# Optimization experiments

Hardware: AMD Instinct MI355X
Metric: run time of the kernel (lower is better)

## Reference

```python
import jax, jax.numpy as jnp
import numpy as np

B, T, H, W = 32, 100, 16, 16
CIN, HID, COUT, K = 64, 128, 64, 5
EPS = 1e-3      # keras LayerNormalization default epsilon
ALPHA = 0.2     # LeakyReLU slope


def _conv_same(x, w):
    # x: [B,H,W,Cin], w: [kh,kw,Cin,Cout] -> [B,H,W,Cout], SAME padding, stride 1
    return jax.lax.conv_general_dilated(
        x, w, window_strides=(1, 1), padding='SAME',
        dimension_numbers=('NHWC', 'HWIO', 'NHWC'))


def setup_inputs() -> dict:
    key = jax.random.key(0)
    ks = jax.random.split(key, 8)
    s = 0.05
    return {
        'initial_input': jax.random.normal(ks[0], (B, 1, H, W, CIN), jnp.float32),
        'h0': jax.random.normal(ks[1], (B, H, W, HID), jnp.float32) * s,
        'c0': jax.random.normal(ks[2], (B, H, W, HID), jnp.float32) * s,
        'targets': jax.random.normal(ks[3], (B, T, H, W, CIN), jnp.float32),
        'autoreg_prob': jnp.float32(0.5),
        # ConvLSTM2D params (keras gate order: i, f, c, o stacked on last axis)
        'Wx': jax.random.normal(ks[4], (K, K, CIN, 4 * HID), jnp.float32) * s,
        'Wh': jax.random.normal(ks[5], (K, K, HID, 4 * HID), jnp.float32) * s,
        'b': jnp.zeros((4 * HID,), jnp.float32),
        # Conv2D(64, 3, same)
        'conv_w': jax.random.normal(ks[6], (3, 3, HID, COUT), jnp.float32) * s,
        'conv_b': jnp.zeros((COUT,), jnp.float32),
        # LayerNorm (axis=-1)
        'gamma': jnp.ones((COUT,), jnp.float32),
        'beta': jnp.zeros((COUT,), jnp.float32),
    }


def reference(initial_input, h0, c0, targets, autoreg_prob,
              Wx, Wh, b, conv_w, conv_b, gamma, beta):
    T_ = targets.shape[1]
    t_switch = jnp.float32(T_) * autoreg_prob
    x0 = initial_input[:, 0]                       # [B,H,W,CIN] (seq-len-1 ConvLSTM step)
    tgt_t = jnp.transpose(targets, (1, 0, 2, 3, 4))  # [T,B,H,W,CIN]
    ts = jnp.arange(T_)

    def step(carry, inp):
        x, h, c = carry
        t, tgt = inp
        # ConvLSTM2D cell (one timestep)
        g = _conv_same(x, Wx) + _conv_same(h, Wh) + b   # [B,H,W,4*HID]
        i_g, f_g, c_g, o_g = jnp.split(g, 4, axis=-1)
        c = jax.nn.sigmoid(f_g) * c + jax.nn.sigmoid(i_g) * jnp.tanh(c_g)
        h = jax.nn.sigmoid(o_g) * jnp.tanh(c)
        # Conv2D -> LayerNorm(axis=-1) -> LeakyReLU(0.2)
        y = _conv_same(h, conv_w) + conv_b              # [B,H,W,COUT]
        mu = jnp.mean(y, axis=-1, keepdims=True)
        var = jnp.var(y, axis=-1, keepdims=True)
        y = (y - mu) * jax.lax.rsqrt(var + EPS) * gamma + beta
        out = jnp.where(y >= 0, y, ALPHA * y)
        # autoreg phase feeds output back; teacher phase feeds targets[:, t]
        next_x = jnp.where(t.astype(jnp.float32) < t_switch, out, tgt)
        return (next_x, h, c), out

    _, outs = jax.lax.scan(step, (x0, h0, c0), (ts, tgt_t))
    return jnp.transpose(outs, (1, 0, 2, 3, 4))        # [B,T,H,W,COUT]
```

## Files before the change

### kernel.cpp

```cpp
#include <hip/hip_runtime.h>

#define TT   100
#define PADW 20
#define HID  128
#define CIN  64
#define COUT 64
#define ALPHA 0.2f
#define LNEPS 1e-3f

typedef _Float16 f16;
typedef __attribute__((ext_vector_type(8))) _Float16 f16x8;
typedef __attribute__((ext_vector_type(4))) float f32x4;

__device__ __forceinline__ float fsig(float x) {
  return __builtin_amdgcn_rcpf(1.f + __builtin_amdgcn_exp2f(-1.44269504089f * x));
}
__device__ __forceinline__ float ftanh(float x) {
  return 1.f - 2.f * __builtin_amdgcn_rcpf(1.f + __builtin_amdgcn_exp2f(2.88539008178f * x));
}
__device__ __forceinline__ void gload16(const void* g, void* l) {
  __builtin_amdgcn_global_load_lds((const __attribute__((address_space(1))) void*)g,
                                   (__attribute__((address_space(3))) void*)l,
                                   16, 0, 0);
}

__global__ __launch_bounds__(512, 1) void kA(
    const f16* __restrict__ Xh, const f16* __restrict__ Xl,
    const f16* __restrict__ Hch, const f16* __restrict__ Hcl,
    f16* __restrict__ Hnh, f16* __restrict__ Hnl,
    const f16* __restrict__ Wch, const f16* __restrict__ Wcl,
    const float* __restrict__ bp, float* __restrict__ cst) {
  __shared__ __align__(16) f16 sAh[2][128][64];
  __shared__ __align__(16) f16 sAl[2][128][64];
  __shared__ __align__(16) f16 sBh[2][128][64];
  __shared__ __align__(16) f16 sBl[2][128][64];
  const int tid = threadIdx.x;
  const int l = tid & 63, w = tid >> 6;
  const int wm = w >> 2, wn = w & 3;
  const int xcd = blockIdx.x & 7, slot = blockIdx.x >> 3;
  const int ni = xcd >> 1;
  const int mi = ((xcd & 1) << 5) + slot;
  const int cof = ((l & 7) ^ (l >> 3)) * 8;

  int posA[2], wBo[2];
#pragma unroll
  for (int i = 0; i < 2; ++i) {
    const int r = w * 16 + i * 8 + (l >> 3);
    const int m = mi * 128 + r;
    const int b = m >> 8, y = (m >> 4) & 15, x = m & 15;
    posA[i] = (b * PADW + y + 2) * PADW + (x + 2);
    wBo[i] = (ni * 128 + r) * 192 + cof;
  }

  auto stage = [&](int bf, int it) {
    const int tap = it / 3, sub = it - tap * 3;
    const int dy = tap / 5, dx = tap - dy * 5;
    const int dt = (dy - 2) * PADW + (dx - 2);
    if (sub == 0) {
#pragma unroll
      for (int i = 0; i < 2; ++i) {
        gload16(Xh + (posA[i] + dt) * CIN + cof, &sAh[bf][w * 16 + i * 8][0]);
        gload16(Xl + (posA[i] + dt) * CIN + cof, &sAl[bf][w * 16 + i * 8][0]);
      }
    } else {
      const int ho = (sub - 1) * 64 + cof;
#pragma unroll
      for (int i = 0; i < 2; ++i) {
        gload16(Hch + (posA[i] + dt) * HID + ho, &sAh[bf][w * 16 + i * 8][0]);
        gload16(Hcl + (posA[i] + dt) * HID + ho, &sAl[bf][w * 16 + i * 8][0]);
      }
    }
    const int wo = tap * (512 * 192) + sub * 64;
#pragma unroll
    for (int i = 0; i < 2; ++i) {
      gload16(Wch + wBo[i] + wo, &sBh[bf][w * 16 + i * 8][0]);
      gload16(Wcl + wBo[i] + wo, &sBl[bf][w * 16 + i * 8][0]);
    }
  };

  f32x4 acc[4][2] = {};

  stage(0, 0);
  __syncthreads();

  int buf = 0;
  for (int it = 0; it < 75; ++it) {
    if (it < 74) stage(buf ^ 1, it + 1);
#pragma unroll
    for (int kk = 0; kk < 2; ++kk) {
      const int co = ((kk * 4 + (l >> 4)) ^ (l & 7)) * 8;
      f16x8 avh[4], avl[4], bvh[2], bvl[2];
#pragma unroll
      for (int fm = 0; fm < 4; ++fm) {
        avh[fm] = *(const f16x8*)&sAh[buf][wm * 64 + fm * 16 + (l & 15)][co];
        avl[fm] = *(const f16x8*)&sAl[buf][wm * 64 + fm * 16 + (l & 15)][co];
      }
#pragma unroll
      for (int fn = 0; fn < 2; ++fn) {
        bvh[fn] = *(const f16x8*)&sBh[buf][wn * 32 + fn * 16 + (l & 15)][co];
        bvl[fn] = *(const f16x8*)&sBl[buf][wn * 32 + fn * 16 + (l & 15)][co];
      }
#pragma unroll
      for (int fm = 0; fm < 4; ++fm)
#pragma unroll
        for (int fn = 0; fn < 2; ++fn) {
          acc[fm][fn] =
              __builtin_amdgcn_mfma_f32_16x16x32_f16(avh[fm], bvh[fn], acc[fm][fn], 0, 0, 0);
          acc[fm][fn] =
              __builtin_amdgcn_mfma_f32_16x16x32_f16(avl[fm], bvh[fn], acc[fm][fn], 0, 0, 0);
          acc[fm][fn] =
              __builtin_amdgcn_mfma_f32_16x16x32_f16(avh[fm], bvl[fn], acc[fm][fn], 0, 0, 0);
        }
    }
    __syncthreads();
    buf ^= 1;
  }

#pragma unroll
  for (int fn = 0; fn < 2; ++fn) {
    const int col = ni * 128 + wn * 32 + fn * 16 + (l & 15);
    const float bias = bp[col];
    const int ch = col >> 2;
#pragma unroll
    for (int fm = 0; fm < 4; ++fm) {
#pragma unroll
      for (int j = 0; j < 4; ++j) {
        const float v = acc[fm][fn][j] + bias;
        const float t1 = __shfl_xor(v, 1);
        const float t2 = __shfl_xor(v, 2);
        const float t3 = __shfl_xor(t1, 2);
        if ((l & 3) == 0) {
          const int m = mi * 128 + wm * 64 + fm * 16 + ((l >> 4) << 2) + j;
          const int cidx = m * HID + ch;
          const float cold = cst[cidx];
          const float cn = fsig(t1) * cold + fsig(v) * ftanh(t2);
          cst[cidx] = cn;
          const float h = fsig(t3) * ftanh(cn);
          const int b = m >> 8, y = (m >> 4) & 15, x = m & 15;
          const int pidx = ((b * PADW + y + 2) * PADW + (x + 2)) * HID + ch;
          const f16 hh = (f16)h;
          Hnh[pidx] = hh;
          Hnl[pidx] = (f16)(h - (float)hh);
        }
      }
    }
  }
}

__global__ __launch_bounds__(256, 2) void kB(
    const f16* __restrict__ Hnh, const f16* __restrict__ Hnl,
    const f16* __restrict__ Cwh, const f16* __restrict__ Cwl,
    const float* __restrict__ cb, const float* __restrict__ gam,
    const float* __restrict__ bet, const float* __restrict__ tgt,
    const float* __restrict__ prob, float* __restrict__ outp,
    f16* __restrict__ Xph, f16* __restrict__ Xpl, int t) {
  __shared__ __align__(16) f16 sAh[2][32][64];
  __shared__ __align__(16) f16 sAl[2][32][64];
  __shared__ __align__(16) f16 sBh[2][64][64];
  __shared__ __align__(16) f16 sBl[2][64][64];
  __shared__ __align__(16) float yl[32][68];
  const int tid = threadIdx.x;
  const int l = tid & 63, w = tid >> 6;
  const int wm = w >> 1, wn = w & 1;
  const int mi = blockIdx.x;
  const int cof = ((l & 7) ^ (l >> 3)) * 8;

  const int rA = w * 8 + (l >> 3);
  const int mA = mi * 32 + rA;
  const int bA = mA >> 8, yA = (mA >> 4) & 15, xA = mA & 15;
  const int posA = (bA * PADW + yA + 2) * PADW + (xA + 2);
  int wBo[2];
#pragma unroll
  for (int i = 0; i < 2; ++i) wBo[i] = (w * 16 + i * 8 + (l >> 3)) * HID + cof;

  auto stage = [&](int bf, int it) {
    const int tap = it >> 1, sub = it & 1;
    const int dy = tap / 3, dx = tap - dy * 3;
    const int dt = (dy - 1) * PADW + (dx - 1);
    gload16(Hnh + (posA + dt) * HID + sub * 64 + cof, &sAh[bf][w * 8][0]);
    gload16(Hnl + (posA + dt) * HID + sub * 64 + cof, &sAl[bf][w * 8][0]);
    const int wo = tap * (64 * HID) + sub * 64;
#pragma unroll
    for (int i = 0; i < 2; ++i) {
      gload16(Cwh + wBo[i] + wo, &sBh[bf][w * 16 + i * 8][0]);
      gload16(Cwl + wBo[i] + wo, &sBl[bf][w * 16 + i * 8][0]);
    }
  };

  f32x4 acc[2] = {};

  stage(0, 0);
  __syncthreads();

  int buf = 0;
  for (int it = 0; it < 18; ++it) {
    if (it < 17) stage(buf ^ 1, it + 1);
#pragma unroll
    for (int kk = 0; kk < 2; ++kk) {
      const int co = ((kk * 4 + (l >> 4)) ^ (l & 7)) * 8;
      const f16x8 ah = *(const f16x8*)&sAh[buf][wm * 16 + (l & 15)][co];
      const f16x8 al = *(const f16x8*)&sAl[buf][wm * 16 + (l & 15)][co];
#pragma unroll
      for (int fn = 0; fn < 2; ++fn) {
        const f16x8 bh = *(const f16x8*)&sBh[buf][wn * 32 + fn * 16 + (l & 15)][co];
        const f16x8 bl = *(const f16x8*)&sBl[buf][wn * 32 + fn * 16 + (l & 15)][co];
        acc[fn] = __builtin_amdgcn_mfma_f32_16x16x32_f16(ah, bh, acc[fn], 0, 0, 0);
        acc[fn] = __builtin_amdgcn_mfma_f32_16x16x32_f16(al, bh, acc[fn], 0, 0, 0);
        acc[fn] = __builtin_amdgcn_mfma_f32_16x16x32_f16(ah, bl, acc[fn], 0, 0, 0);
      }
    }
    __syncthreads();
    buf ^= 1;
  }

#pragma unroll
  for (int fn = 0; fn < 2; ++fn) {
    const int col = wn * 32 + fn * 16 + (l & 15);
    const float bias = cb[col];
#pragma unroll
    for (int j = 0; j < 4; ++j) yl[wm * 16 + (l >> 4) * 4 + j][col] = acc[fn][j] + bias;
  }
  __syncthreads();

  if (tid < 128) {
    const int row = tid >> 2, part = tid & 3;
    f32x4 vv[4];
    float s = 0.f, q = 0.f;
#pragma unroll
    for (int k2 = 0; k2 < 4; ++k2) {
      vv[k2] = *(const f32x4*)&yl[row][part * 16 + k2 * 4];
#pragma unroll
      for (int e = 0; e < 4; ++e) { const float f = vv[k2][e]; s += f; q += f * f; }
    }
    s += __shfl_xor(s, 1); q += __shfl_xor(q, 1);
    s += __shfl_xor(s, 2); q += __shfl_xor(q, 2);
    const float mean = s * 0.015625f;
    const float var = q * 0.015625f - mean * mean;
    const float rs = __builtin_amdgcn_rsqf(fmaxf(var, 0.f) + LNEPS);
    const int m = mi * 32 + row;
    const int b = m >> 8, pos = m & 255;
    const int py = pos >> 4, px = pos & 15;
    const long obase = (((long)b * TT + t) * 256 + pos) * COUT + part * 16;
    float* op = outp + obase;
    const float* tp = tgt + obase;
    const bool ar = (float)t < 100.f * prob[0];
    const int xoff = ((b * PADW + py + 2) * PADW + px + 2) * CIN + part * 16;
    f16x8 ph[2], pl[2];
#pragma unroll
    for (int k2 = 0; k2 < 4; ++k2) {
      f32x4 o4;
#pragma unroll
      for (int e = 0; e < 4; ++e) {
        const int c = part * 16 + k2 * 4 + e;
        float val = (vv[k2][e] - mean) * rs * gam[c] + bet[c];
        val = val >= 0.f ? val : ALPHA * val;
        o4[e] = val;
        const float nxt = ar ? val : tp[k2 * 4 + e];
        const f16 nh = (f16)nxt;
        const int i16 = k2 * 4 + e;
        ph[i16 >> 3][i16 & 7] = nh;
        pl[i16 >> 3][i16 & 7] = (f16)(nxt - (float)nh);
      }
      *(f32x4*)(op + k2 * 4) = o4;
    }
    *(f16x8*)(Xph + xoff) = ph[0];
    *(f16x8*)(Xph + xoff + 8) = ph[1];
    *(f16x8*)(Xpl + xoff) = pl[0];
    *(f16x8*)(Xpl + xoff + 8) = pl[1];
  }
}

__global__ void k_wcomb(const float* __restrict__ Wx, const float* __restrict__ Wh,
                        f16* __restrict__ Wch, f16* __restrict__ Wcl) {
  const int idx = blockIdx.x * 256 + threadIdx.x;
  if (idx >= 25 * 512 * 192) return;
  const int c = idx % 192, r = idx / 192;
  const int n = r % 512, tap = r / 512;
  const int ch = n >> 2, g = n & 3, no = g * 128 + ch;
  const float v = (c < 64) ? Wx[(tap * 64 + c) * 512 + no]
                           : Wh[(tap * 128 + (c - 64)) * 512 + no];
  const f16 vh = (f16)v;
  Wch[idx] = vh;
  Wcl[idx] = (f16)(v - (float)vh);
}
__global__ void k_wconv(const float* __restrict__ cw, f16* __restrict__ Cwh,
                        f16* __restrict__ Cwl) {
  const int idx = blockIdx.x * 256 + threadIdx.x;
  if (idx >= 9 * 64 * 128) return;
  const int c = idx % 128, r = idx / 128;
  const int n = r % 64, tap = r / 64;
  const float v = cw[(tap * 128 + c) * 64 + n];
  const f16 vh = (f16)v;
  Cwh[idx] = vh;
  Cwl[idx] = (f16)(v - (float)vh);
}
__global__ void k_bperm(const float* __restrict__ b, float* __restrict__ bp) {
  const int n = blockIdx.x * 256 + threadIdx.x;
  if (n < 512) bp[n] = b[(n & 3) * 128 + (n >> 2)];
}
__global__ void k_init(const float* __restrict__ x0, const float* __restrict__ h0,
                       const float* __restrict__ c0, f16* __restrict__ Xph,
                       f16* __restrict__ Xpl, f16* __restrict__ Hh, f16* __restrict__ Hl,
                       float* __restrict__ cst) {
  const int idx = blockIdx.x * 256 + threadIdx.x;
  if (idx < 32 * 256 * 64) {
    const int ch = idx & 63, m = idx >> 6;
    const int b = m >> 8, y = (m >> 4) & 15, x = m & 15;
    const int p = ((b * PADW + y + 2) * PADW + x + 2) * CIN + ch;
    const float v = x0[idx];
    const f16 vh = (f16)v;
    Xph[p] = vh;
    Xpl[p] = (f16)(v - (float)vh);
  } else if (idx < 32 * 256 * 64 + 32 * 256 * 128) {
    const int j = idx - 32 * 256 * 64;
    const int ch = j & 127, m = j >> 7;
    const int b = m >> 8, y = (m >> 4) & 15, x = m & 15;
    const int p = ((b * PADW + y + 2) * PADW + x + 2) * HID + ch;
    const float v = h0[j];
    const f16 vh = (f16)v;
    Hh[p] = vh;
    Hl[p] = (f16)(v - (float)vh);
  } else if (idx < 32 * 256 * 64 + 2 * 32 * 256 * 128) {
    const int j = idx - 32 * 256 * 64 - 32 * 256 * 128;
    cst[j] = c0[j];
  }
}

extern "C" void kernel_launch(void* const* d_in, const int* in_sizes, int n_in,
                              void* d_out, int out_size, void* d_ws, size_t ws_size,
                              hipStream_t stream) {
  (void)in_sizes; (void)n_in; (void)out_size; (void)ws_size;
  const float* x0  = (const float*)d_in[0];
  const float* h0  = (const float*)d_in[1];
  const float* c0  = (const float*)d_in[2];
  const float* tgt = (const float*)d_in[3];
  const float* pr  = (const float*)d_in[4];
  const float* Wx  = (const float*)d_in[5];
  const float* Wh  = (const float*)d_in[6];
  const float* bb  = (const float*)d_in[7];
  const float* cw  = (const float*)d_in[8];
  const float* cbv = (const float*)d_in[9];
  const float* gam = (const float*)d_in[10];
  const float* bet = (const float*)d_in[11];
  float* outp = (float*)d_out;
  char* ws = (char*)d_ws;
  f16*   Xph = (f16*)(ws + 0);
  f16*   Xpl = (f16*)(ws + 1638400);
  f16*   Hh0 = (f16*)(ws + 3276800);
  f16*   Hl0 = (f16*)(ws + 6553600);
  f16*   Hh1 = (f16*)(ws + 9830400);
  f16*   Hl1 = (f16*)(ws + 13107200);
  float* cst = (float*)(ws + 16384000);
  f16*   Wch = (f16*)(ws + 20578304);
  f16*   Wcl = (f16*)(ws + 25493504);
  f16*   Cwh = (f16*)(ws + 30408704);
  f16*   Cwl = (f16*)(ws + 30556160);
  float* bp  = (float*)(ws + 30703616);

  hipMemsetAsync(Xph, 0, 1638400, stream);
  hipMemsetAsync(Xpl, 0, 1638400, stream);
  hipMemsetAsync(Hh0, 0, 3276800, stream);
  hipMemsetAsync(Hl0, 0, 3276800, stream);
  hipMemsetAsync(Hh1, 0, 3276800, stream);
  hipMemsetAsync(Hl1, 0, 3276800, stream);
  k_wcomb<<<9600, 256, 0, stream>>>(Wx, Wh, Wch, Wcl);
  k_wconv<<<288, 256, 0, stream>>>(cw, Cwh, Cwl);
  k_bperm<<<2, 256, 0, stream>>>(bb, bp);
  k_init<<<10240, 256, 0, stream>>>(x0, h0, c0, Xph, Xpl, Hh0, Hl0, cst);

  for (int t = 0; t < TT; ++t) {
    f16* hch = (t & 1) ? Hh1 : Hh0;
    f16* hcl = (t & 1) ? Hl1 : Hl0;
    f16* hnh = (t & 1) ? Hh0 : Hh1;
    f16* hnl = (t & 1) ? Hl0 : Hl1;
    kA<<<256, 512, 0, stream>>>(Xph, Xpl, hch, hcl, hnh, hnl, Wch, Wcl, bp, cst);
    kB<<<256, 256, 0, stream>>>(hnh, hnl, Cwh, Cwl, cbv, gam, bet, tgt, pr, outp, Xph, Xpl, t);
  }
}
```

Baseline: 14.70 ms.

## Enlarge gate-GEMM tile to 128x256 and split K across two blocks

The ConvLSTM gate GEMM now uses a 128x256 output tile with K-chunks of 32, which raises operand reuse per LDS load. The reduction is split in two halves across separate blocks that write fp32 partial sums, and a new elementwise kernel adds them, applies the bias and runs the LSTM cell update. This keeps 256 blocks in flight despite the larger tiles. The cost is an extra kernel launch per timestep and the write and read of two 16MB partial buffers. If the workspace is too small it falls back to a single-block K loop over 128 blocks.

```diff
diff --git a/kernel.cpp b/kernel.cpp
--- a/kernel.cpp
+++ b/kernel.cpp
@@ -24,127 +24,162 @@
                                    16, 0, 0);
 }
 
-__global__ __launch_bounds__(512, 1) void kA(
+__global__ __launch_bounds__(512, 2) void kA2(
     const f16* __restrict__ Xh, const f16* __restrict__ Xl,
     const f16* __restrict__ Hch, const f16* __restrict__ Hcl,
-    f16* __restrict__ Hnh, f16* __restrict__ Hnl,
     const f16* __restrict__ Wch, const f16* __restrict__ Wcl,
-    const float* __restrict__ bp, float* __restrict__ cst) {
-  __shared__ __align__(16) f16 sAh[2][128][64];
-  __shared__ __align__(16) f16 sAl[2][128][64];
-  __shared__ __align__(16) f16 sBh[2][128][64];
-  __shared__ __align__(16) f16 sBl[2][128][64];
+    float* __restrict__ P0, float* __restrict__ P1,
+    f16* __restrict__ Hnh, f16* __restrict__ Hnl, float* __restrict__ cst,
+    const float* __restrict__ bp, int nsplit) {
+  __shared__ __align__(16) f16 sAh[2][128][32];
+  __shared__ __align__(16) f16 sAl[2][128][32];
+  __shared__ __align__(16) f16 sBh[2][256][32];
+  __shared__ __align__(16) f16 sBl[2][256][32];
   const int tid = threadIdx.x;
   const int l = tid & 63, w = tid >> 6;
   const int wm = w >> 2, wn = w & 3;
-  const int xcd = blockIdx.x & 7, slot = blockIdx.x >> 3;
-  const int ni = xcd >> 1;
-  const int mi = ((xcd & 1) << 5) + slot;
-  const int cof = ((l & 7) ^ (l >> 3)) * 8;
-
-  int posA[2], wBo[2];
-#pragma unroll
-  for (int i = 0; i < 2; ++i) {
-    const int r = w * 16 + i * 8 + (l >> 3);
-    const int m = mi * 128 + r;
-    const int b = m >> 8, y = (m >> 4) & 15, x = m & 15;
-    posA[i] = (b * PADW + y + 2) * PADW + (x + 2);
-    wBo[i] = (ni * 128 + r) * 192 + cof;
-  }
-
-  auto stage = [&](int bf, int it) {
-    const int tap = it / 3, sub = it - tap * 3;
+
+  int tm, tn, ks;
+  {
+    const int xcd = blockIdx.x & 7, slot = blockIdx.x >> 3;
+    tn = xcd >> 2;
+    if (nsplit == 2) { ks = (xcd >> 1) & 1; tm = ((xcd & 1) << 5) | slot; }
+    else             { ks = 0;             tm = ((xcd & 3) << 4) | slot; }
+  }
+  const int sub0 = ks * 75;
+  const int nsub = (nsplit == 2) ? 75 : 150;
+
+  const int arow = tid >> 2;
+  const int gch = ((tid & 3) ^ ((tid >> 3) & 3)) * 8;
+  const int mA = tm * 128 + arow;
+  const int bA = mA >> 8, yA = (mA >> 4) & 15, xA = mA & 15;
+  const int posA = (bA * PADW + yA + 2) * PADW + (xA + 2);
+  const int nB0 = (tn * 256 + arow) * 192;
+  const int nB1 = (tn * 256 + 128 + arow) * 192;
+
+  auto stage = [&](int bf, int s) {
+    const int tap = s / 6, r = s - tap * 6;
     const int dy = tap / 5, dx = tap - dy * 5;
     const int dt = (dy - 2) * PADW + (dx - 2);
-    if (sub == 0) {
-#pragma unroll
-      for (int i = 0; i < 2; ++i) {
-        gload16(Xh + (posA[i] + dt) * CIN + cof, &sAh[bf][w * 16 + i * 8][0]);
-        gload16(Xl + (posA[i] + dt) * CIN + cof, &sAl[bf][w * 16 + i * 8][0]);
+    if (r < 2) {
+      const int off = (posA + dt) * CIN + r * 32 + gch;
+      gload16(Xh + off, &sAh[bf][w * 16][0]);
+      gload16(Xl + off, &sAl[bf][w * 16][0]);
+    } else {
+      const int off = (posA + dt) * HID + (r - 2) * 32 + gch;
+      gload16(Hch + off, &sAh[bf][w * 16][0]);
+      gload16(Hcl + off, &sAl[bf][w * 16][0]);
+    }
+    const int wo = tap * (512 * 192) + r * 32 + gch;
+    gload16(Wch + wo + nB0, &sBh[bf][w * 16][0]);
+    gload16(Wcl + wo + nB0, &sBl[bf][w * 16][0]);
+    gload16(Wch + wo + nB1, &sBh[bf][128 + w * 16][0]);
+    gload16(Wcl + wo + nB1, &sBl[bf][128 + w * 16][0]);
+  };
+
+  f32x4 acc[4][4] = {};
+
+  stage(0, sub0);
+  __syncthreads();
+
+  const int sl = ((l & 15) >> 1) & 3;
+  const int kc = (((l >> 4) ^ sl)) * 8;
+
+  int buf = 0;
+  for (int it = 0; it < nsub; ++it) {
+    if (it < nsub - 1) stage(buf ^ 1, sub0 + it + 1);
+    f16x8 avh[4], avl[4], bvh[4], bvl[4];
+#pragma unroll
+    for (int fm = 0; fm < 4; ++fm) {
+      avh[fm] = *(const f16x8*)&sAh[buf][wm * 64 + fm * 16 + (l & 15)][kc];
+      avl[fm] = *(const f16x8*)&sAl[buf][wm * 64 + fm * 16 + (l & 15)][kc];
+    }
+#pragma unroll
+    for (int fn = 0; fn < 4; ++fn) {
+      bvh[fn] = *(const f16x8*)&sBh[buf][wn * 64 + fn * 16 + (l & 15)][kc];
+      bvl[fn] = *(const f16x8*)&sBl[buf][wn * 64 + fn * 16 + (l & 15)][kc];
+    }
+#pragma unroll
+    for (int fm = 0; fm < 4; ++fm)
+#pragma unroll
+      for (int fn = 0; fn < 4; ++fn) {
+        acc[fm][fn] =
+            __builtin_amdgcn_mfma_f32_16x16x32_f16(avh[fm], bvh[fn], acc[fm][fn], 0, 0, 0);
+        acc[fm][fn] =
+            __builtin_amdgcn_mfma_f32_16x16x32_f16(avl[fm], bvh[fn], acc[fm][fn], 0, 0, 0);
+        acc[fm][fn] =
+            __builtin_amdgcn_mfma_f32_16x16x32_f16(avh[fm], bvl[fn], acc[fm][fn], 0, 0, 0);
       }
-    } else {
-      const int ho = (sub - 1) * 64 + cof;
-#pragma unroll
-      for (int i = 0; i < 2; ++i) {
-        gload16(Hch + (posA[i] + dt) * HID + ho, &sAh[bf][w * 16 + i * 8][0]);
-        gload16(Hcl + (posA[i] + dt) * HID + ho, &sAl[bf][w * 16 + i * 8][0]);
-      }
-    }
-    const int wo = tap * (512 * 192) + sub * 64;
-#pragma unroll
-    for (int i = 0; i < 2; ++i) {
-      gload16(Wch + wBo[i] + wo, &sBh[bf][w * 16 + i * 8][0]);
-      gload16(Wcl + wBo[i] + wo, &sBl[bf][w * 16 + i * 8][0]);
-    }
-  };
-
-  f32x4 acc[4][2] = {};
-
-  stage(0, 0);
-  __syncthreads();
-
-  int buf = 0;
-  for (int it = 0; it < 75; ++it) {
-    if (it < 74) stage(buf ^ 1, it + 1);
-#pragma unroll
-    for (int kk = 0; kk < 2; ++kk) {
-      const int co = ((kk * 4 + (l >> 4)) ^ (l & 7)) * 8;
-      f16x8 avh[4], avl[4], bvh[2], bvl[2];
-#pragma unroll
-      for (int fm = 0; fm < 4; ++fm) {
-        avh[fm] = *(const f16x8*)&sAh[buf][wm * 64 + fm * 16 + (l & 15)][co];
-        avl[fm] = *(const f16x8*)&sAl[buf][wm * 64 + fm * 16 + (l & 15)][co];
-      }
-#pragma unroll
-      for (int fn = 0; fn < 2; ++fn) {
-        bvh[fn] = *(const f16x8*)&sBh[buf][wn * 32 + fn * 16 + (l & 15)][co];
-        bvl[fn] = *(const f16x8*)&sBl[buf][wn * 32 + fn * 16 + (l & 15)][co];
-      }
-#pragma unroll
-      for (int fm = 0; fm < 4; ++fm)
-#pragma unroll
-        for (int fn = 0; fn < 2; ++fn) {
-          acc[fm][fn] =
-              __builtin_amdgcn_mfma_f32_16x16x32_f16(avh[fm], bvh[fn], acc[fm][fn], 0, 0, 0);
-          acc[fm][fn] =
-              __builtin_amdgcn_mfma_f32_16x16x32_f16(avl[fm], bvh[fn], acc[fm][fn], 0, 0, 0);
-          acc[fm][fn] =
-              __builtin_amdgcn_mfma_f32_16x16x32_f16(avh[fm], bvl[fn], acc[fm][fn], 0, 0, 0);
-        }
-    }
     __syncthreads();
     buf ^= 1;
   }
 
-#pragma unroll
-  for (int fn = 0; fn < 2; ++fn) {
-    const int col = ni * 128 + wn * 32 + fn * 16 + (l & 15);
-    const float bias = bp[col];
-    const int ch = col >> 2;
-#pragma unroll
-    for (int fm = 0; fm < 4; ++fm) {
+  if (nsplit == 2) {
+    float* __restrict__ P = ks ? P1 : P0;
+#pragma unroll
+    for (int fm = 0; fm < 4; ++fm)
 #pragma unroll
       for (int j = 0; j < 4; ++j) {
-        const float v = acc[fm][fn][j] + bias;
-        const float t1 = __shfl_xor(v, 1);
-        const float t2 = __shfl_xor(v, 2);
-        const float t3 = __shfl_xor(t1, 2);
-        if ((l & 3) == 0) {
-          const int m = mi * 128 + wm * 64 + fm * 16 + ((l >> 4) << 2) + j;
-          const int cidx = m * HID + ch;
-          const float cold = cst[cidx];
-          const float cn = fsig(t1) * cold + fsig(v) * ftanh(t2);
-          cst[cidx] = cn;
-          const float h = fsig(t3) * ftanh(cn);
-          const int b = m >> 8, y = (m >> 4) & 15, x = m & 15;
-          const int pidx = ((b * PADW + y + 2) * PADW + (x + 2)) * HID + ch;
-          const f16 hh = (f16)h;
-          Hnh[pidx] = hh;
-          Hnl[pidx] = (f16)(h - (float)hh);
+        const int row = tm * 128 + wm * 64 + fm * 16 + ((l >> 4) << 2) + j;
+        float* pr = P + (long)row * 512 + tn * 256 + wn * 64 + (l & 15);
+#pragma unroll
+        for (int fn = 0; fn < 4; ++fn) pr[fn * 16] = acc[fm][fn][j];
+      }
+  } else {
+#pragma unroll
+    for (int fn = 0; fn < 4; ++fn) {
+      const int col = tn * 256 + wn * 64 + fn * 16 + (l & 15);
+      const float bias = bp[col];
+      const int ch = col >> 2;
+#pragma unroll
+      for (int fm = 0; fm < 4; ++fm) {
+#pragma unroll
+        for (int j = 0; j < 4; ++j) {
+          const float v = acc[fm][fn][j] + bias;
+          const float t1 = __shfl_xor(v, 1);
+          const float t2 = __shfl_xor(v, 2);
+          const float t3 = __shfl_xor(t1, 2);
+          if ((l & 3) == 0) {
+            const int m = tm * 128 + wm * 64 + fm * 16 + ((l >> 4) << 2) + j;
+            const int cidx = m * HID + ch;
+            const float cold = cst[cidx];
+            const float cn = fsig(t1) * cold + fsig(v) * ftanh(t2);
+            cst[cidx] = cn;
+            const float h = fsig(t3) * ftanh(cn);
+            const int b = m >> 8, y = (m >> 4) & 15, x = m & 15;
+            const int pidx = ((b * PADW + y + 2) * PADW + (x + 2)) * HID + ch;
+            const f16 hh = (f16)h;
+            Hnh[pidx] = hh;
+            Hnl[pidx] = (f16)(h - (float)hh);
+          }
         }
       }
     }
   }
+}
+
+__global__ __launch_bounds__(256) void kE(
+    const float* __restrict__ P0, const float* __restrict__ P1,
+    const float* __restrict__ bp, float* __restrict__ cst,
+    f16* __restrict__ Hnh, f16* __restrict__ Hnl) {
+  const int tid = threadIdx.x;
+  const int m = blockIdx.x * 2 + (tid >> 7), ch = tid & 127;
+  const f32x4 a = *(const f32x4*)&P0[(long)m * 512 + ch * 4];
+  const f32x4 c4 = *(const f32x4*)&P1[(long)m * 512 + ch * 4];
+  const f32x4 bi = *(const f32x4*)&bp[ch * 4];
+  const float ig = a[0] + c4[0] + bi[0];
+  const float fg = a[1] + c4[1] + bi[1];
+  const float cg = a[2] + c4[2] + bi[2];
+  const float og = a[3] + c4[3] + bi[3];
+  const int cidx = m * HID + ch;
+  const float cn = fsig(fg) * cst[cidx] + fsig(ig) * ftanh(cg);
+  cst[cidx] = cn;
+  const float h = fsig(og) * ftanh(cn);
+  const int b = m >> 8, y = (m >> 4) & 15, x = m & 15;
+  const int pidx = ((b * PADW + y + 2) * PADW + (x + 2)) * HID + ch;
+  const f16 hh = (f16)h;
+  Hnh[pidx] = hh;
+  Hnl[pidx] = (f16)(h - (float)hh);
 }
 
 __global__ __launch_bounds__(256, 2) void kB(
@@ -329,7 +364,7 @@
 extern "C" void kernel_launch(void* const* d_in, const int* in_sizes, int n_in,
                               void* d_out, int out_size, void* d_ws, size_t ws_size,
                               hipStream_t stream) {
-  (void)in_sizes; (void)n_in; (void)out_size; (void)ws_size;
+  (void)in_sizes; (void)n_in; (void)out_size;
   const float* x0  = (const float*)d_in[0];
   const float* h0  = (const float*)d_in[1];
   const float* c0  = (const float*)d_in[2];
@@ -356,6 +391,10 @@
   f16*   Cwh = (f16*)(ws + 30408704);
   f16*   Cwl = (f16*)(ws + 30556160);
   float* bp  = (float*)(ws + 30703616);
+  float* P0  = (float*)(ws + 30705664);
+  float* P1  = (float*)(ws + 47482880);
+  const size_t NEED = 47482880ull + 16777216ull;
+  const int nsplit = (ws_size >= NEED) ? 2 : 1;
 
   hipMemsetAsync(Xph, 0, 1638400, stream);
   hipMemsetAsync(Xpl, 0, 1638400, stream);
@@ -373,7 +412,14 @@
     f16* hcl = (t & 1) ? Hl1 : Hl0;
     f16* hnh = (t & 1) ? Hh0 : Hh1;
     f16* hnl = (t & 1) ? Hl0 : Hl1;
-    kA<<<256, 512, 0, stream>>>(Xph, Xpl, hch, hcl, hnh, hnl, Wch, Wcl, bp, cst);
+    if (nsplit == 2) {
+      kA2<<<256, 512, 0, stream>>>(Xph, Xpl, hch, hcl, Wch, Wcl, P0, P1,
+                                   hnh, hnl, cst, bp, 2);
+      kE<<<4096, 256, 0, stream>>>(P0, P1, bp, cst, hnh, hnl);
+    } else {
+      kA2<<<128, 512, 0, stream>>>(Xph, Xpl, hch, hcl, Wch, Wcl, P0, P1,
+                                   hnh, hnl, cst, bp, 1);
+    }
     kB<<<256, 256, 0, stream>>>(hnh, hnl, Cwh, Cwl, cbv, gam, bet, tgt, pr, outp, Xph, Xpl, t);
   }
 }
```

New measurement: 17.12 ms. 1.16x slower.

## Triple-buffer gate GEMM with 4 waves, 64x64 warp tiles and vmcnt waits

Applied to the files above, without the earlier changes.

The ConvLSTM gate GEMM kernel goes from 8 waves with a 2-stage, K=64 LDS pipeline to 4 waves with a 3-stage, K=32 pipeline. Each wave now computes a 64x64 tile instead of 64x32, which improves LDS-fragment reuse per MFMA. Partial s_waitcnt vmcnt plus raw s_barrier let loads stay in flight across iterations instead of draining fully at __syncthreads. The conv kernel kB gets the same waitcnt/barrier treatment. The cost is fewer waves per CU for latency hiding and higher accumulator register pressure.

```diff
diff --git a/kernel.cpp b/kernel.cpp
--- a/kernel.cpp
+++ b/kernel.cpp
@@ -24,101 +24,102 @@
                                    16, 0, 0);
 }
 
-__global__ __launch_bounds__(512, 1) void kA(
+__global__ __launch_bounds__(256, 1) void kA3(
     const f16* __restrict__ Xh, const f16* __restrict__ Xl,
     const f16* __restrict__ Hch, const f16* __restrict__ Hcl,
     f16* __restrict__ Hnh, f16* __restrict__ Hnl,
     const f16* __restrict__ Wch, const f16* __restrict__ Wcl,
     const float* __restrict__ bp, float* __restrict__ cst) {
-  __shared__ __align__(16) f16 sAh[2][128][64];
-  __shared__ __align__(16) f16 sAl[2][128][64];
-  __shared__ __align__(16) f16 sBh[2][128][64];
-  __shared__ __align__(16) f16 sBl[2][128][64];
+  __shared__ __align__(16) f16 sAh[3][128][32];
+  __shared__ __align__(16) f16 sAl[3][128][32];
+  __shared__ __align__(16) f16 sBh[3][128][32];
+  __shared__ __align__(16) f16 sBl[3][128][32];
   const int tid = threadIdx.x;
   const int l = tid & 63, w = tid >> 6;
-  const int wm = w >> 2, wn = w & 3;
-  const int xcd = blockIdx.x & 7, slot = blockIdx.x >> 3;
-  const int ni = xcd >> 1;
-  const int mi = ((xcd & 1) << 5) + slot;
-  const int cof = ((l & 7) ^ (l >> 3)) * 8;
+  const int wm = w >> 1, wn = w & 1;
+  const int xcd = blockIdx.x & 7;
+  const int tn = xcd >> 1;
+  const int tm = ((xcd & 1) << 5) | (blockIdx.x >> 3);
+  const int gch = ((l & 3) ^ ((l >> 3) & 3)) * 8;
 
   int posA[2], wBo[2];
 #pragma unroll
   for (int i = 0; i < 2; ++i) {
-    const int r = w * 16 + i * 8 + (l >> 3);
-    const int m = mi * 128 + r;
+    const int r = w * 32 + i * 16 + (l >> 2);
+    const int m = tm * 128 + r;
     const int b = m >> 8, y = (m >> 4) & 15, x = m & 15;
     posA[i] = (b * PADW + y + 2) * PADW + (x + 2);
-    wBo[i] = (ni * 128 + r) * 192 + cof;
-  }
-
-  auto stage = [&](int bf, int it) {
-    const int tap = it / 3, sub = it - tap * 3;
+    wBo[i] = (tn * 128 + r) * 192 + gch;
+  }
+
+  auto stage = [&](int bf, int s) {
+    const int tap = s / 6, r6 = s - tap * 6;
     const int dy = tap / 5, dx = tap - dy * 5;
     const int dt = (dy - 2) * PADW + (dx - 2);
-    if (sub == 0) {
+    if (r6 < 2) {
+      const int co = r6 * 32 + gch;
 #pragma unroll
       for (int i = 0; i < 2; ++i) {
-        gload16(Xh + (posA[i] + dt) * CIN + cof, &sAh[bf][w * 16 + i * 8][0]);
-        gload16(Xl + (posA[i] + dt) * CIN + cof, &sAl[bf][w * 16 + i * 8][0]);
+        gload16(Xh + (posA[i] + dt) * CIN + co, &sAh[bf][w * 32 + i * 16][0]);
+        gload16(Xl + (posA[i] + dt) * CIN + co, &sAl[bf][w * 32 + i * 16][0]);
       }
     } else {
-      const int ho = (sub - 1) * 64 + cof;
+      const int co = (r6 - 2) * 32 + gch;
 #pragma unroll
       for (int i = 0; i < 2; ++i) {
-        gload16(Hch + (posA[i] + dt) * HID + ho, &sAh[bf][w * 16 + i * 8][0]);
-        gload16(Hcl + (posA[i] + dt) * HID + ho, &sAl[bf][w * 16 + i * 8][0]);
-      }
-    }
-    const int wo = tap * (512 * 192) + sub * 64;
+        gload16(Hch + (posA[i] + dt) * HID + co, &sAh[bf][w * 32 + i * 16][0]);
+        gload16(Hcl + (posA[i] + dt) * HID + co, &sAl[bf][w * 32 + i * 16][0]);
+      }
+    }
+    const int wo = tap * (512 * 192) + r6 * 32;
 #pragma unroll
     for (int i = 0; i < 2; ++i) {
-      gload16(Wch + wBo[i] + wo, &sBh[bf][w * 16 + i * 8][0]);
-      gload16(Wcl + wBo[i] + wo, &sBl[bf][w * 16 + i * 8][0]);
+      gload16(Wch + wo + wBo[i], &sBh[bf][w * 32 + i * 16][0]);
+      gload16(Wcl + wo + wBo[i], &sBl[bf][w * 32 + i * 16][0]);
     }
   };
 
-  f32x4 acc[4][2] = {};
-
+  f32x4 acc[4][4] = {};
   stage(0, 0);
-  __syncthreads();
-
-  int buf = 0;
-  for (int it = 0; it < 75; ++it) {
-    if (it < 74) stage(buf ^ 1, it + 1);
-#pragma unroll
-    for (int kk = 0; kk < 2; ++kk) {
-      const int co = ((kk * 4 + (l >> 4)) ^ (l & 7)) * 8;
-      f16x8 avh[4], avl[4], bvh[2], bvl[2];
-#pragma unroll
-      for (int fm = 0; fm < 4; ++fm) {
-        avh[fm] = *(const f16x8*)&sAh[buf][wm * 64 + fm * 16 + (l & 15)][co];
-        avl[fm] = *(const f16x8*)&sAl[buf][wm * 64 + fm * 16 + (l & 15)][co];
-      }
-#pragma unroll
-      for (int fn = 0; fn < 2; ++fn) {
-        bvh[fn] = *(const f16x8*)&sBh[buf][wn * 32 + fn * 16 + (l & 15)][co];
-        bvl[fn] = *(const f16x8*)&sBl[buf][wn * 32 + fn * 16 + (l & 15)][co];
-      }
-#pragma unroll
-      for (int fm = 0; fm < 4; ++fm)
-#pragma unroll
-        for (int fn = 0; fn < 2; ++fn) {
-          acc[fm][fn] =
-              __builtin_amdgcn_mfma_f32_16x16x32_f16(avh[fm], bvh[fn], acc[fm][fn], 0, 0, 0);
-          acc[fm][fn] =
-              __builtin_amdgcn_mfma_f32_16x16x32_f16(avl[fm], bvh[fn], acc[fm][fn], 0, 0, 0);
-          acc[fm][fn] =
-              __builtin_amdgcn_mfma_f32_16x16x32_f16(avh[fm], bvl[fn], acc[fm][fn], 0, 0, 0);
-        }
-    }
-    __syncthreads();
-    buf ^= 1;
-  }
-
-#pragma unroll
-  for (int fn = 0; fn < 2; ++fn) {
-    const int col = ni * 128 + wn * 32 + fn * 16 + (l & 15);
+  stage(1, 1);
+
+  const int kc = ((l >> 4) ^ (((l & 15) >> 1) & 3)) * 8;
+  int cur = 0;
+  for (int s = 0; s < 150; ++s) {
+    int bn = cur + 2; if (bn >= 3) bn -= 3;
+    stage(bn, (s + 2 < 150) ? s + 2 : 149);
+    asm volatile("s_waitcnt vmcnt(16)" ::: "memory");
+    __builtin_amdgcn_s_barrier();
+    f16x8 avh[4], avl[4], bvh[4], bvl[4];
+#pragma unroll
+    for (int fm = 0; fm < 4; ++fm) {
+      avh[fm] = *(const f16x8*)&sAh[cur][wm * 64 + fm * 16 + (l & 15)][kc];
+      avl[fm] = *(const f16x8*)&sAl[cur][wm * 64 + fm * 16 + (l & 15)][kc];
+    }
+#pragma unroll
+    for (int fn = 0; fn < 4; ++fn) {
+      bvh[fn] = *(const f16x8*)&sBh[cur][wn * 64 + fn * 16 + (l & 15)][kc];
+      bvl[fn] = *(const f16x8*)&sBl[cur][wn * 64 + fn * 16 + (l & 15)][kc];
+    }
+#pragma unroll
+    for (int fm = 0; fm < 4; ++fm)
+#pragma unroll
+      for (int fn = 0; fn < 4; ++fn) {
+        acc[fm][fn] =
+            __builtin_amdgcn_mfma_f32_16x16x32_f16(avh[fm], bvh[fn], acc[fm][fn], 0, 0, 0);
+        acc[fm][fn] =
+            __builtin_amdgcn_mfma_f32_16x16x32_f16(avl[fm], bvh[fn], acc[fm][fn], 0, 0, 0);
+        acc[fm][fn] =
+            __builtin_amdgcn_mfma_f32_16x16x32_f16(avh[fm], bvl[fn], acc[fm][fn], 0, 0, 0);
+      }
+    asm volatile("s_waitcnt lgkmcnt(0)" ::: "memory");
+    __builtin_amdgcn_s_barrier();
+    cur = (cur == 2) ? 0 : cur + 1;
+  }
+
+#pragma unroll
+  for (int fn = 0; fn < 4; ++fn) {
+    const int col = tn * 128 + wn * 64 + fn * 16 + (l & 15);
     const float bias = bp[col];
     const int ch = col >> 2;
 #pragma unroll
@@ -130,7 +131,7 @@
         const float t2 = __shfl_xor(v, 2);
         const float t3 = __shfl_xor(t1, 2);
         if ((l & 3) == 0) {
-          const int m = mi * 128 + wm * 64 + fm * 16 + ((l >> 4) << 2) + j;
+          const int m = tm * 128 + wm * 64 + fm * 16 + ((l >> 4) << 2) + j;
           const int cidx = m * HID + ch;
           const float cold = cst[cidx];
           const float cn = fsig(t1) * cold + fsig(v) * ftanh(t2);
@@ -188,13 +189,13 @@
   };
 
   f32x4 acc[2] = {};
-
   stage(0, 0);
-  __syncthreads();
 
   int buf = 0;
   for (int it = 0; it < 18; ++it) {
-    if (it < 17) stage(buf ^ 1, it + 1);
+    stage(buf ^ 1, (it + 1 < 18) ? it + 1 : 17);
+    asm volatile("s_waitcnt vmcnt(6)" ::: "memory");
+    __builtin_amdgcn_s_barrier();
 #pragma unroll
     for (int kk = 0; kk < 2; ++kk) {
       const int co = ((kk * 4 + (l >> 4)) ^ (l & 7)) * 8;
@@ -209,7 +210,8 @@
         acc[fn] = __builtin_amdgcn_mfma_f32_16x16x32_f16(ah, bl, acc[fn], 0, 0, 0);
       }
     }
-    __syncthreads();
+    asm volatile("s_waitcnt lgkmcnt(0)" ::: "memory");
+    __builtin_amdgcn_s_barrier();
     buf ^= 1;
   }
 
@@ -373,7 +375,7 @@
     f16* hcl = (t & 1) ? Hl1 : Hl0;
     f16* hnh = (t & 1) ? Hh0 : Hh1;
     f16* hnl = (t & 1) ? Hl0 : Hl1;
-    kA<<<256, 512, 0, stream>>>(Xph, Xpl, hch, hcl, hnh, hnl, Wch, Wcl, bp, cst);
+    kA3<<<256, 256, 0, stream>>>(Xph, Xpl, hch, hcl, hnh, hnl, Wch, Wcl, bp, cst);
     kB<<<256, 256, 0, stream>>>(hnh, hnl, Cwh, Cwl, cbv, gam, bet, tgt, pr, outp, Xph, Xpl, t);
   }
 }
```

Measured after the change: 34.38 ms. 134% more time.

## Split K across wave pairs in gate GEMM with LDS reduction

Applied to the files above, without the earlier changes.

Each wave now computes a larger 64x64 output subtile over half of each 64-wide K slice, instead of a 64x32 subtile over the full slice. Pairs of waves then reduce their partial accumulators through shared memory before the LSTM epilogue. This raises MFMA work per LDS fragment load, cutting shared-memory read traffic per MFMA. The cost is twice the accumulator registers, an extra LDS round trip and barrier, and an epilogue run by only half the waves.

```diff
diff --git a/kernel.cpp b/kernel.cpp
--- a/kernel.cpp
+++ b/kernel.cpp
@@ -24,19 +24,23 @@
                                    16, 0, 0);
 }
 
-__global__ __launch_bounds__(512, 1) void kA(
+__global__ __launch_bounds__(512, 1) void kA6(
     const f16* __restrict__ Xh, const f16* __restrict__ Xl,
     const f16* __restrict__ Hch, const f16* __restrict__ Hcl,
     f16* __restrict__ Hnh, f16* __restrict__ Hnl,
     const f16* __restrict__ Wch, const f16* __restrict__ Wcl,
     const float* __restrict__ bp, float* __restrict__ cst) {
-  __shared__ __align__(16) f16 sAh[2][128][64];
-  __shared__ __align__(16) f16 sAl[2][128][64];
-  __shared__ __align__(16) f16 sBh[2][128][64];
-  __shared__ __align__(16) f16 sBl[2][128][64];
+  __shared__ __align__(16) char smem[131072];
+  f16 (*sAh)[128][64] = (f16(*)[128][64])(smem);
+  f16 (*sAl)[128][64] = (f16(*)[128][64])(smem + 32768);
+  f16 (*sBh)[128][64] = (f16(*)[128][64])(smem + 65536);
+  f16 (*sBl)[128][64] = (f16(*)[128][64])(smem + 98304);
+  float* macc = (float*)smem;
+
   const int tid = threadIdx.x;
   const int l = tid & 63, w = tid >> 6;
-  const int wm = w >> 2, wn = w & 3;
+  const int h = w & 1, q = w >> 1;
+  const int qm = q >> 1, qn = q & 1;
   const int xcd = blockIdx.x & 7, slot = blockIdx.x >> 3;
   const int ni = xcd >> 1;
   const int mi = ((xcd & 1) << 5) + slot;
@@ -78,69 +82,87 @@
     }
   };
 
-  f32x4 acc[4][2] = {};
+  f32x4 acc[4][4] = {};
 
   stage(0, 0);
   __syncthreads();
+
+  const int co = ((h * 4 + (l >> 4)) ^ (l & 7)) * 8;
 
   int buf = 0;
   for (int it = 0; it < 75; ++it) {
     if (it < 74) stage(buf ^ 1, it + 1);
-#pragma unroll
-    for (int kk = 0; kk < 2; ++kk) {
-      const int co = ((kk * 4 + (l >> 4)) ^ (l & 7)) * 8;
-      f16x8 avh[4], avl[4], bvh[2], bvl[2];
-#pragma unroll
-      for (int fm = 0; fm < 4; ++fm) {
-        avh[fm] = *(const f16x8*)&sAh[buf][wm * 64 + fm * 16 + (l & 15)][co];
-        avl[fm] = *(const f16x8*)&sAl[buf][wm * 64 + fm * 16 + (l & 15)][co];
-      }
-#pragma unroll
-      for (int fn = 0; fn < 2; ++fn) {
-        bvh[fn] = *(const f16x8*)&sBh[buf][wn * 32 + fn * 16 + (l & 15)][co];
-        bvl[fn] = *(const f16x8*)&sBl[buf][wn * 32 + fn * 16 + (l & 15)][co];
-      }
-#pragma unroll
-      for (int fm = 0; fm < 4; ++fm)
-#pragma unroll
-        for (int fn = 0; fn < 2; ++fn) {
-          acc[fm][fn] =
-              __builtin_amdgcn_mfma_f32_16x16x32_f16(avh[fm], bvh[fn], acc[fm][fn], 0, 0, 0);
-          acc[fm][fn] =
-              __builtin_amdgcn_mfma_f32_16x16x32_f16(avl[fm], bvh[fn], acc[fm][fn], 0, 0, 0);
-          acc[fm][fn] =
-              __builtin_amdgcn_mfma_f32_16x16x32_f16(avh[fm], bvl[fn], acc[fm][fn], 0, 0, 0);
-        }
-    }
+    f16x8 avh[4], avl[4], bvh[4], bvl[4];
+#pragma unroll
+    for (int fm = 0; fm < 4; ++fm) {
+      avh[fm] = *(const f16x8*)&sAh[buf][qm * 64 + fm * 16 + (l & 15)][co];
+      avl[fm] = *(const f16x8*)&sAl[buf][qm * 64 + fm * 16 + (l & 15)][co];
+    }
+#pragma unroll
+    for (int fn = 0; fn < 4; ++fn) {
+      bvh[fn] = *(const f16x8*)&sBh[buf][qn * 64 + fn * 16 + (l & 15)][co];
+      bvl[fn] = *(const f16x8*)&sBl[buf][qn * 64 + fn * 16 + (l & 15)][co];
+    }
+#pragma unroll
+    for (int fm = 0; fm < 4; ++fm)
+#pragma unroll
+      for (int fn = 0; fn < 4; ++fn) {
+        acc[fm][fn] =
+            __builtin_amdgcn_mfma_f32_16x16x32_f16(avh[fm], bvh[fn], acc[fm][fn], 0, 0, 0);
+        acc[fm][fn] =
+            __builtin_amdgcn_mfma_f32_16x16x32_f16(avl[fm], bvh[fn], acc[fm][fn], 0, 0, 0);
+        acc[fm][fn] =
+            __builtin_amdgcn_mfma_f32_16x16x32_f16(avh[fm], bvl[fn], acc[fm][fn], 0, 0, 0);
+      }
     __syncthreads();
     buf ^= 1;
   }
 
-#pragma unroll
-  for (int fn = 0; fn < 2; ++fn) {
-    const int col = ni * 128 + wn * 32 + fn * 16 + (l & 15);
-    const float bias = bp[col];
-    const int ch = col >> 2;
-#pragma unroll
-    for (int fm = 0; fm < 4; ++fm) {
-#pragma unroll
-      for (int j = 0; j < 4; ++j) {
-        const float v = acc[fm][fn][j] + bias;
-        const float t1 = __shfl_xor(v, 1);
-        const float t2 = __shfl_xor(v, 2);
-        const float t3 = __shfl_xor(t1, 2);
-        if ((l & 3) == 0) {
-          const int m = mi * 128 + wm * 64 + fm * 16 + ((l >> 4) << 2) + j;
-          const int cidx = m * HID + ch;
-          const float cold = cst[cidx];
-          const float cn = fsig(t1) * cold + fsig(v) * ftanh(t2);
-          cst[cidx] = cn;
-          const float h = fsig(t3) * ftanh(cn);
-          const int b = m >> 8, y = (m >> 4) & 15, x = m & 15;
-          const int pidx = ((b * PADW + y + 2) * PADW + (x + 2)) * HID + ch;
-          const f16 hh = (f16)h;
-          Hnh[pidx] = hh;
-          Hnl[pidx] = (f16)(h - (float)hh);
+  if (h == 1) {
+#pragma unroll
+    for (int fm = 0; fm < 4; ++fm)
+#pragma unroll
+      for (int fn = 0; fn < 4; ++fn)
+#pragma unroll
+        for (int j = 0; j < 4; ++j)
+          macc[q * 4096 + ((fm * 4 + fn) * 4 + j) * 64 + l] = acc[fm][fn][j];
+  }
+  __syncthreads();
+  if (h == 0) {
+#pragma unroll
+    for (int fm = 0; fm < 4; ++fm)
+#pragma unroll
+      for (int fn = 0; fn < 4; ++fn)
+#pragma unroll
+        for (int j = 0; j < 4; ++j)
+          acc[fm][fn][j] += macc[q * 4096 + ((fm * 4 + fn) * 4 + j) * 64 + l];
+
+#pragma unroll
+    for (int fn = 0; fn < 4; ++fn) {
+      const int col = ni * 128 + qn * 64 + fn * 16 + (l & 15);
+      const float bias = bp[col];
+      const int ch = col >> 2;
+#pragma unroll
+      for (int fm = 0; fm < 4; ++fm) {
+#pragma unroll
+        for (int j = 0; j < 4; ++j) {
+          const float v = acc[fm][fn][j] + bias;
+          const float t1 = __shfl_xor(v, 1);
+          const float t2 = __shfl_xor(v, 2);
+          const float t3 = __shfl_xor(t1, 2);
+          if ((l & 3) == 0) {
+            const int m = mi * 128 + qm * 64 + fm * 16 + ((l >> 4) << 2) + j;
+            const int cidx = m * HID + ch;
+            const float cold = cst[cidx];
+            const float cn = fsig(t1) * cold + fsig(v) * ftanh(t2);
+            cst[cidx] = cn;
+            const float hh_ = fsig(t3) * ftanh(cn);
+            const int b = m >> 8, y = (m >> 4) & 15, x = m & 15;
+            const int pidx = ((b * PADW + y + 2) * PADW + (x + 2)) * HID + ch;
+            const f16 hv = (f16)hh_;
+            Hnh[pidx] = hv;
+            Hnl[pidx] = (f16)(hh_ - (float)hv);
+          }
         }
       }
     }
@@ -373,7 +395,7 @@
     f16* hcl = (t & 1) ? Hl1 : Hl0;
     f16* hnh = (t & 1) ? Hh0 : Hh1;
     f16* hnl = (t & 1) ? Hl0 : Hl1;
-    kA<<<256, 512, 0, stream>>>(Xph, Xpl, hch, hcl, hnh, hnl, Wch, Wcl, bp, cst);
+    kA6<<<256, 512, 0, stream>>>(Xph, Xpl, hch, hcl, hnh, hnl, Wch, Wcl, bp, cst);
     kB<<<256, 256, 0, stream>>>(hnh, hnl, Cwh, Cwl, cbv, gam, bet, tgt, pr, outp, Xph, Xpl, t);
   }
 }
```

Result: faster. 13.81 ms (-6.0%).
